# Kernel optimization log

Hardware: AMD Instinct MI355X
Metric: run time of the kernel (lower is better)

## Reference

```python
import jax, jax.numpy as jnp
import numpy as np

C = 4          # num_components
B = 2          # true batch
HEADS = 24
DIM_HEAD = 64
D = HEADS * DIM_HEAD      # 1536, attn.out_dim == query dim
CROSS = 2048              # encoder hidden dim
S = 2048                  # latent sequence length
E = 77                    # encoder sequence length
PAD = 77                  # pad_length (must equal E for the broadcast in the original code)


def setup_inputs() -> dict:
    key = jax.random.key(0)
    ks = jax.random.split(key, 12)
    w = 0.02
    return {
        "hidden_states": jax.random.normal(ks[0], (B * C, S, D), jnp.float32),
        "encoder_hidden_states": jax.random.normal(ks[1], (B * C, E, CROSS), jnp.float32),
        "Wq": jax.random.normal(ks[2], (D, D), jnp.float32) * w,
        "bq": jax.random.normal(ks[3], (D,), jnp.float32) * w,
        "Wk": jax.random.normal(ks[4], (D, CROSS), jnp.float32) * w,
        "bk": jax.random.normal(ks[5], (D,), jnp.float32) * w,
        "Wv": jax.random.normal(ks[6], (D, CROSS), jnp.float32) * w,
        "bv": jax.random.normal(ks[7], (D,), jnp.float32) * w,
        "Wo": jax.random.normal(ks[8], (D, D), jnp.float32) * w,
        "bo": jax.random.normal(ks[9], (D,), jnp.float32) * w,
        "pad_length": PAD,
    }


def reference(hidden_states, encoder_hidden_states, Wq, bq, Wk, bk, Wv, bv, Wo, bo, pad_length):
    BC, S_, D_ = hidden_states.shape
    E_ = encoder_hidden_states.shape[1]
    Bsz = BC // C
    scale = 1.0 / np.sqrt(DIM_HEAD)

    # projections (torch nn.Linear: x @ W.T + b)
    q = hidden_states @ Wq.T + bq                      # [BC, S, D]
    k = encoder_hidden_states @ Wk.T + bk              # [BC, E, D]
    v = encoder_hidden_states @ Wv.T + bv              # [BC, E, D]
    # pad branch: to_k/to_v applied to zeros -> just the bias, broadcast over pad tokens
    k_pad = jnp.broadcast_to(bk, (BC, pad_length, D_))  # [BC, PAD, D]
    v_pad = jnp.broadcast_to(bv, (BC, pad_length, D_))
    v = jnp.concatenate([v, v_pad], axis=1)            # [BC, E+PAD, D]

    # split heads
    qh = q.reshape(BC, S_, HEADS, DIM_HEAD)
    kh = k.reshape(BC, E_, HEADS, DIM_HEAD)
    kph = k_pad.reshape(BC, pad_length, HEADS, DIM_HEAD)
    vh = v.reshape(BC, E_ + pad_length, HEADS, DIM_HEAD)

    # scores: [BC, H, S, E] and [BC, H, S, PAD]
    scores = jnp.einsum("bihd,bjhd->bhij", qh, kh) * scale
    scores_pad = jnp.einsum("bihd,bjhd->bhij", qh, kph) * scale

    # component-wise softmax: view as [C, B, H, S, *], softmax over component axis 0
    scores = scores.reshape(C, Bsz, HEADS, S_, E_)
    scores_pad = scores_pad.reshape(C, Bsz, HEADS, S_, pad_length)
    w_main = jax.nn.softmax(scores, axis=0)
    w_pad = jax.nn.softmax(scores_pad, axis=0) * (C / pad_length) * (1.0 - w_main)

    w_main = w_main.reshape(BC, HEADS, S_, E_)
    w_pad = w_pad.reshape(BC, HEADS, S_, pad_length)
    weights = jnp.concatenate([w_main, w_pad], axis=-1)  # [BC, H, S, E+PAD]

    # attention @ V -> merge heads
    out = jnp.einsum("bhij,bjhd->bihd", weights, vh).reshape(BC, S_, D_)
    out = out @ Wo.T + bo   # to_out[0]; dropout is identity in eval
    return out
```

## Files before the change

kernel.cpp:

```cpp
#include <hip/hip_runtime.h>
#include <hip/hip_bf16.h>


typedef __attribute__((ext_vector_type(8))) short short8;
typedef __attribute__((ext_vector_type(4))) float f32x4;
typedef __attribute__((ext_vector_type(4))) _Float16 half4;

#define DEV __device__ __forceinline__

DEV ushort f2bf(float x) {
  __hip_bfloat16 h = __float2bfloat16(x);
  return *reinterpret_cast<ushort*>(&h);
}


__global__ __launch_bounds__(256) void cvt_f32_bf16(const float* __restrict__ in,
                                                    ushort* __restrict__ out, int n4) {
  int idx = blockIdx.x * blockDim.x + threadIdx.x;
  int stride = gridDim.x * blockDim.x;
  for (int q = idx; q < n4; q += stride) {
    float4 f = reinterpret_cast<const float4*>(in)[q];
    ushort4 o;
    o.x = f2bf(f.x); o.y = f2bf(f.y); o.z = f2bf(f.z); o.w = f2bf(f.w);
    reinterpret_cast<ushort4*>(out)[q] = o;
  }
}

__global__ __launch_bounds__(256) void cvt_pad_ehs(const float* __restrict__ in,
                                                   ushort* __restrict__ out) {
  int q = blockIdx.x * blockDim.x + threadIdx.x;
  if (q >= 640 * 2048 / 4) return;
  int r = (q * 4) >> 11;
  ushort4 o;
  if (r < 616) {
    float4 f = reinterpret_cast<const float4*>(in)[q];
    o.x = f2bf(f.x); o.y = f2bf(f.y); o.z = f2bf(f.z); o.w = f2bf(f.w);
  } else {
    o.x = 0; o.y = 0; o.z = 0; o.w = 0;
  }
  reinterpret_cast<ushort4*>(out)[q] = o;
}


template <typename OutT>
__global__ __launch_bounds__(256) void gemm_p(const ushort* __restrict__ A,
                                              const ushort* __restrict__ B,
                                              const float* __restrict__ bias,
                                              OutT* __restrict__ C, int M, int N, int K) {
  __shared__ __align__(16) ushort lds[32768];
  const int tid = threadIdx.x;
  const int lane = tid & 63;
  const int wid = tid >> 6;
  const int wr = wid >> 1, wc = wid & 1;
  const long m0 = (long)blockIdx.x * 128;
  const long n0 = (long)blockIdx.y * 128;
  const int ll = lane & 15, g = lane >> 4;
  const int swz = ll & 7;

  const int srow = wid * 8 + (lane >> 3);
  const int scol = ((lane & 7) ^ (lane >> 3)) * 8;
  const ushort* pa = A + (m0 + srow) * (long)K + scol;
  const ushort* pb = B + (n0 + srow) * (long)K + scol;
  const long qstep = 32 * (long)K;

  f32x4 acc[4][4] = {};

#define STAGE(tt, bsel)                                                                    \
  do {                                                                                     \
    const long kt_ = (long)(tt) * 64;                                                      \
    const int ab_ = (bsel) * 32768 + wid * 1024;                                           \
    _Pragma("unroll") for (int q = 0; q < 4; ++q)                                          \
        __builtin_amdgcn_global_load_lds(                                                  \
            (const __attribute__((address_space(1))) void*)(pa + kt_ + q * qstep),         \
            (__attribute__((address_space(3))) void*)((char*)lds + ab_ + q * 4096),        \
            16, 0, 0);                                                                     \
    _Pragma("unroll") for (int q = 0; q < 4; ++q)                                          \
        __builtin_amdgcn_global_load_lds(                                                  \
            (const __attribute__((address_space(1))) void*)(pb + kt_ + q * qstep),         \
            (__attribute__((address_space(3))) void*)((char*)lds + ab_ + 16384 + q * 4096),\
            16, 0, 0);                                                                     \
  } while (0)

  const int nt = K >> 6;
  STAGE(0, 0);
  STAGE(1, 1);
  asm volatile("s_waitcnt vmcnt(8)" ::: "memory");
  __builtin_amdgcn_s_barrier();

  for (int t = 0; t < nt; ++t) {
    const int buf = t & 1;
    const char* abase = (const char*)lds + buf * 32768;
    const char* bbase = abase + 16384;
    short8 af[4][2], bfr[4][2];
#pragma unroll
    for (int m = 0; m < 4; ++m)
#pragma unroll
      for (int ks = 0; ks < 2; ++ks)
        af[m][ks] = *reinterpret_cast<const short8*>(
            abase + (wr * 64 + m * 16 + ll) * 128 + (((ks * 4 + g) ^ swz) * 16));
#pragma unroll
    for (int n = 0; n < 4; ++n)
#pragma unroll
      for (int ks = 0; ks < 2; ++ks)
        bfr[n][ks] = *reinterpret_cast<const short8*>(
            bbase + (wc * 64 + n * 16 + ll) * 128 + (((ks * 4 + g) ^ swz) * 16));
    asm volatile("s_waitcnt lgkmcnt(0)" ::: "memory");
    __builtin_amdgcn_s_barrier();

    if (t < nt - 2) {
      STAGE(t + 2, buf);
      asm volatile("s_waitcnt vmcnt(8)" ::: "memory");
    } else if (t == nt - 2) {
      asm volatile("s_waitcnt vmcnt(0)" ::: "memory");
    }
    __builtin_amdgcn_sched_barrier(0);
    __builtin_amdgcn_s_setprio(1);
#pragma unroll
    for (int ks = 0; ks < 2; ++ks)
#pragma unroll
      for (int m = 0; m < 4; ++m)
#pragma unroll
        for (int n = 0; n < 4; ++n)
          acc[m][n] =
              __builtin_amdgcn_mfma_f32_16x16x32_bf16(af[m][ks], bfr[n][ks], acc[m][n], 0, 0, 0);
    __builtin_amdgcn_s_setprio(0);
    __builtin_amdgcn_s_barrier();
  }
#undef STAGE

#pragma unroll
  for (int m = 0; m < 4; ++m) {
#pragma unroll
    for (int n = 0; n < 4; ++n) {
      const int row = wr * 64 + m * 16 + g * 4;
      const int col = wc * 64 + n * 16 + ll;
      const float bias_v = bias[n0 + col];
#pragma unroll
      for (int r = 0; r < 4; ++r) {
        float val = acc[m][n][r] + bias_v;
        long off = (m0 + row + r) * (long)N + n0 + col;
        if constexpr (sizeof(OutT) == 2) {
          C[off] = (OutT)f2bf(val);
        } else {
          C[off] = val;
        }
      }
    }
  }
}


__global__ __launch_bounds__(256) void attn_v2(const ushort* __restrict__ qg,
                                               const float* __restrict__ kg,
                                               const float* __restrict__ vg,
                                               const float* __restrict__ bk,
                                               const float* __restrict__ bv,
                                               ushort* __restrict__ ao) {
  __shared__ __align__(16) ushort kl[4 * 80 * 64];
  __shared__ __align__(16) _Float16 vt[4 * 64 * 80];
  const int tid = threadIdx.x;
  const int lane = tid & 63;
  const int w = tid >> 6;
  const int h = blockIdx.y, bb = blockIdx.z;
  const int i0 = blockIdx.x * 64;

  for (int rr = tid; rr < 320; rr += 256) {
    int c = rr / 80, j = rr - c * 80;
    ushort* krow = &kl[c * 5120 + j * 64];
    _Float16* vcol = &vt[c * 5120 + j];
    const int swz = j & 7;
    if (j < 77) {
      const float* ksrc = kg + ((long)((c * 2 + bb) * 77 + j)) * 1536 + h * 64;
      const float* vsrc = vg + ((long)((c * 2 + bb) * 77 + j)) * 1536 + h * 64;
#pragma unroll
      for (int t = 0; t < 8; ++t) {
        float4 f0 = reinterpret_cast<const float4*>(ksrc)[2 * t];
        float4 f1 = reinterpret_cast<const float4*>(ksrc)[2 * t + 1];
        short8 v;
        v[0] = f2bf(f0.x); v[1] = f2bf(f0.y); v[2] = f2bf(f0.z); v[3] = f2bf(f0.w);
        v[4] = f2bf(f1.x); v[5] = f2bf(f1.y); v[6] = f2bf(f1.z); v[7] = f2bf(f1.w);
        *reinterpret_cast<short8*>(krow + (t ^ swz) * 8) = v;
      }
#pragma unroll
      for (int d = 0; d < 64; ++d) vcol[d * 80] = (_Float16)vsrc[d];
    } else if (j == 77) {
      const float* ksrc = bk + h * 64;
      const float* vsrc = bv + h * 64;
#pragma unroll
      for (int t = 0; t < 8; ++t) {
        float4 f0 = reinterpret_cast<const float4*>(ksrc)[2 * t];
        float4 f1 = reinterpret_cast<const float4*>(ksrc)[2 * t + 1];
        short8 v;
        v[0] = f2bf(f0.x); v[1] = f2bf(f0.y); v[2] = f2bf(f0.z); v[3] = f2bf(f0.w);
        v[4] = f2bf(f1.x); v[5] = f2bf(f1.y); v[6] = f2bf(f1.z); v[7] = f2bf(f1.w);
        *reinterpret_cast<short8*>(krow + (t ^ swz) * 8) = v;
      }
#pragma unroll
      for (int d = 0; d < 64; ++d) vcol[d * 80] = (_Float16)vsrc[d];
    } else {
      short8 z = {};
#pragma unroll
      for (int t = 0; t < 8; ++t) *reinterpret_cast<short8*>(krow + (t ^ swz) * 8) = z;
#pragma unroll
      for (int d = 0; d < 64; ++d) vcol[d * 80] = (_Float16)0.f;
    }
  }
  __syncthreads();

  const int ll = lane & 15, g = lane >> 4;

  f32x4 s[4][5];
#pragma unroll
  for (int c = 0; c < 4; ++c)
#pragma unroll
    for (int m = 0; m < 5; ++m) s[c][m] = (f32x4){0.f, 0.f, 0.f, 0.f};

#pragma unroll
  for (int c = 0; c < 4; ++c) {
    const ushort* qbase =
        qg + ((long)((c * 2 + bb) * 2048 + i0 + w * 16 + ll)) * 1536 + h * 64 + g * 8;
    short8 qf0 = *reinterpret_cast<const short8*>(qbase);
    short8 qf1 = *reinterpret_cast<const short8*>(qbase + 32);
#pragma unroll
    for (int m = 0; m < 5; ++m) {
      const char* base = (const char*)kl + c * 10240 + (m * 16 + ll) * 128;
      short8 a0 = *reinterpret_cast<const short8*>(base + ((g ^ (ll & 7)) * 16));
      short8 a1 = *reinterpret_cast<const short8*>(base + (((4 + g) ^ (ll & 7)) * 16));
      s[c][m] = __builtin_amdgcn_mfma_f32_16x16x32_bf16(a0, qf0, s[c][m], 0, 0, 0);
      s[c][m] = __builtin_amdgcn_mfma_f32_16x16x32_bf16(a1, qf1, s[c][m], 0, 0, 0);
    }
  }

  const float scale = 0.125f;
  float wsum0 = 0.f, wsum1 = 0.f, wsum2 = 0.f, wsum3 = 0.f;
#pragma unroll
  for (int m = 0; m < 5; ++m) {
#pragma unroll
    for (int e = 0; e < 4; ++e) {
      float x0 = s[0][m][e] * scale, x1 = s[1][m][e] * scale;
      float x2 = s[2][m][e] * scale, x3 = s[3][m][e] * scale;
      float mx = fmaxf(fmaxf(x0, x1), fmaxf(x2, x3));
      float e0 = __expf(x0 - mx), e1 = __expf(x1 - mx);
      float e2 = __expf(x2 - mx), e3 = __expf(x3 - mx);
      float inv = __fdividef(1.f, e0 + e1 + e2 + e3);
      float w0 = e0 * inv, w1 = e1 * inv, w2 = e2 * inv, w3 = e3 * inv;
      int jj = m * 16 + g * 4 + e;
      float msk = (jj < 77) ? 1.f : 0.f;
      wsum0 += w0 * msk; wsum1 += w1 * msk; wsum2 += w2 * msk; wsum3 += w3 * msk;
      s[0][m][e] = w0; s[1][m][e] = w1; s[2][m][e] = w2; s[3][m][e] = w3;
    }
  }
  wsum0 += __shfl_xor(wsum0, 16); wsum0 += __shfl_xor(wsum0, 32);
  wsum1 += __shfl_xor(wsum1, 16); wsum1 += __shfl_xor(wsum1, 32);
  wsum2 += __shfl_xor(wsum2, 16); wsum2 += __shfl_xor(wsum2, 32);
  wsum3 += __shfl_xor(wsum3, 16); wsum3 += __shfl_xor(wsum3, 32);

  const bool g3 = (g == 3);
  {
    float wsum[4] = {wsum0, wsum1, wsum2, wsum3};
#pragma unroll
    for (int c = 0; c < 4; ++c) {
      float w77 = s[c][4][1];
      float pwv = w77 * (4.0f / 77.0f) * (77.0f - wsum[c]);
      s[c][4][1] = g3 ? pwv : w77;
      s[c][4][2] = g3 ? 0.f : s[c][4][2];
      s[c][4][3] = g3 ? 0.f : s[c][4][3];
    }
  }

  half4 wf[4][5];
#pragma unroll
  for (int c = 0; c < 4; ++c)
#pragma unroll
    for (int m = 0; m < 5; ++m) {
      half4 hv;
      hv[0] = (_Float16)s[c][m][0];
      hv[1] = (_Float16)s[c][m][1];
      hv[2] = (_Float16)s[c][m][2];
      hv[3] = (_Float16)s[c][m][3];
      wf[c][m] = hv;
    }

  f32x4 o[4][4];
#pragma unroll
  for (int c = 0; c < 4; ++c)
#pragma unroll
    for (int n = 0; n < 4; ++n) o[c][n] = (f32x4){0.f, 0.f, 0.f, 0.f};

#pragma unroll
  for (int c = 0; c < 4; ++c)
#pragma unroll
    for (int m = 0; m < 5; ++m)
#pragma unroll
      for (int n = 0; n < 4; ++n) {
        half4 vf = *reinterpret_cast<const half4*>(
            &vt[c * 5120 + (n * 16 + ll) * 80 + m * 16 + g * 4]);
        o[c][n] = __builtin_amdgcn_mfma_f32_16x16x16f16(wf[c][m], vf, o[c][n], 0, 0, 0);
      }

#pragma unroll
  for (int c = 0; c < 4; ++c)
#pragma unroll
    for (int n = 0; n < 4; ++n)
#pragma unroll
      for (int r = 0; r < 4; ++r) {
        long row = (long)((c * 2 + bb) * 2048 + i0 + w * 16 + g * 4 + r);
        ao[row * 1536 + h * 64 + n * 16 + ll] = f2bf(o[c][n][r]);
      }
}


extern "C" void kernel_launch(void* const* d_in, const int* in_sizes, int n_in,
                              void* d_out, int out_size, void* d_ws, size_t ws_size,
                              hipStream_t stream) {
  (void)in_sizes; (void)n_in; (void)out_size; (void)ws_size;
  const float* hs  = (const float*)d_in[0];
  const float* ehs = (const float*)d_in[1];
  const float* Wq  = (const float*)d_in[2];
  const float* bq  = (const float*)d_in[3];
  const float* Wk  = (const float*)d_in[4];
  const float* bk  = (const float*)d_in[5];
  const float* Wv  = (const float*)d_in[6];
  const float* bv  = (const float*)d_in[7];
  const float* Wo  = (const float*)d_in[8];
  const float* bo  = (const float*)d_in[9];
  float* out = (float*)d_out;

  char* ws = (char*)d_ws;
  size_t off = 0;
  auto alloc = [&](size_t bytes) {
    char* p = ws + off;
    off += (bytes + 255) & ~(size_t)255;
    return p;
  };
  ushort* hs_bf  = (ushort*)alloc(16384UL * 1536 * 2);
  ushort* ehs_bf = (ushort*)alloc(640UL * 2048 * 2);
  ushort* Wq_bf  = (ushort*)alloc(1536UL * 1536 * 2);
  ushort* Wk_bf  = (ushort*)alloc(1536UL * 2048 * 2);
  ushort* Wv_bf  = (ushort*)alloc(1536UL * 2048 * 2);
  ushort* Wo_bf  = (ushort*)alloc(1536UL * 1536 * 2);
  ushort* q_bf   = (ushort*)alloc(16384UL * 1536 * 2);
  float*  k_f    = (float*)alloc(640UL * 1536 * 4);
  float*  v_f    = (float*)alloc(640UL * 1536 * 4);
  ushort* ao_bf  = (ushort*)alloc(16384UL * 1536 * 2);

  dim3 b256(256);
  cvt_f32_bf16<<<2048, b256, 0, stream>>>(hs, hs_bf, 16384 * 1536 / 4);
  cvt_pad_ehs<<<(640 * 2048 / 4 + 255) / 256, b256, 0, stream>>>(ehs, ehs_bf);
  cvt_f32_bf16<<<1024, b256, 0, stream>>>(Wq, Wq_bf, 1536 * 1536 / 4);
  cvt_f32_bf16<<<1024, b256, 0, stream>>>(Wk, Wk_bf, 1536 * 2048 / 4);
  cvt_f32_bf16<<<1024, b256, 0, stream>>>(Wv, Wv_bf, 1536 * 2048 / 4);
  cvt_f32_bf16<<<1024, b256, 0, stream>>>(Wo, Wo_bf, 1536 * 1536 / 4);

  gemm_p<float><<<dim3(5, 12), b256, 0, stream>>>(ehs_bf, Wk_bf, bk, k_f, 640, 1536, 2048);
  gemm_p<float><<<dim3(5, 12), b256, 0, stream>>>(ehs_bf, Wv_bf, bv, v_f, 640, 1536, 2048);
  gemm_p<ushort><<<dim3(128, 12), b256, 0, stream>>>(hs_bf, Wq_bf, bq, q_bf, 16384, 1536, 1536);
  attn_v2<<<dim3(32, 24, 2), b256, 0, stream>>>(q_bf, k_f, v_f, bk, bv, ao_bf);
  gemm_p<float><<<dim3(128, 12), b256, 0, stream>>>(ao_bf, Wo_bf, bo, out, 16384, 1536, 1536);
}
```

Baseline: 318.1 us.

## Load GEMM B operand directly from global, halve LDS, batch weight conversions

The GEMM now stages only the A tile through LDS and reads the B (weight) fragments straight from global memory into registers. This halves LDS use and sets launch bounds to allow 3 blocks per CU, aiming for higher occupancy. The four weight conversions are merged into one launch, and the K and V projections into one launch, to cut launch overhead. In exchange, every block reads B from global without LDS sharing, and those loads are not coalesced the way the staged loads were, which risks higher memory latency and traffic. The vmcnt wait counts are adjusted for the mix of direct and LDS loads.

```diff
diff --git a/kernel.cpp b/kernel.cpp
--- a/kernel.cpp
+++ b/kernel.cpp
@@ -16,6 +16,27 @@
 
 __global__ __launch_bounds__(256) void cvt_f32_bf16(const float* __restrict__ in,
                                                     ushort* __restrict__ out, int n4) {
+  int idx = blockIdx.x * blockDim.x + threadIdx.x;
+  int stride = gridDim.x * blockDim.x;
+  for (int q = idx; q < n4; q += stride) {
+    float4 f = reinterpret_cast<const float4*>(in)[q];
+    ushort4 o;
+    o.x = f2bf(f.x); o.y = f2bf(f.y); o.z = f2bf(f.z); o.w = f2bf(f.w);
+    reinterpret_cast<ushort4*>(out)[q] = o;
+  }
+}
+
+__global__ __launch_bounds__(256) void cvt_w4(const float* __restrict__ w0, ushort* __restrict__ o0, int m0,
+                                              const float* __restrict__ w1, ushort* __restrict__ o1, int m1,
+                                              const float* __restrict__ w2, ushort* __restrict__ o2, int m2,
+                                              const float* __restrict__ w3, ushort* __restrict__ o3, int m3) {
+  const float* in; ushort* out; int n4;
+  switch (blockIdx.y) {
+    case 0: in = w0; out = o0; n4 = m0; break;
+    case 1: in = w1; out = o1; n4 = m1; break;
+    case 2: in = w2; out = o2; n4 = m2; break;
+    default: in = w3; out = o3; n4 = m3; break;
+  }
   int idx = blockIdx.x * blockDim.x + threadIdx.x;
   int stride = gridDim.x * blockDim.x;
   for (int q = idx; q < n4; q += stride) {
@@ -43,11 +64,10 @@
 
 
 template <typename OutT>
-__global__ __launch_bounds__(256) void gemm_p(const ushort* __restrict__ A,
-                                              const ushort* __restrict__ B,
-                                              const float* __restrict__ bias,
-                                              OutT* __restrict__ C, int M, int N, int K) {
-  __shared__ __align__(16) ushort lds[32768];
+DEV void gemm_body(const ushort* __restrict__ A, const ushort* __restrict__ B,
+                   const float* __restrict__ bias, OutT* __restrict__ C,
+                   int M, int N, int K) {
+  __shared__ __align__(16) ushort lds[16384];
   const int tid = threadIdx.x;
   const int lane = tid & 63;
   const int wid = tid >> 6;
@@ -60,37 +80,31 @@
   const int srow = wid * 8 + (lane >> 3);
   const int scol = ((lane & 7) ^ (lane >> 3)) * 8;
   const ushort* pa = A + (m0 + srow) * (long)K + scol;
-  const ushort* pb = B + (n0 + srow) * (long)K + scol;
   const long qstep = 32 * (long)K;
+  const ushort* pB = B + (n0 + wc * 64 + ll) * (long)K + g * 8;
 
   f32x4 acc[4][4] = {};
 
-#define STAGE(tt, bsel)                                                                    \
+#define STAGEA(tt, bsel)                                                                   \
   do {                                                                                     \
     const long kt_ = (long)(tt) * 64;                                                      \
-    const int ab_ = (bsel) * 32768 + wid * 1024;                                           \
+    const int ab_ = (bsel) * 16384 + wid * 1024;                                           \
     _Pragma("unroll") for (int q = 0; q < 4; ++q)                                          \
         __builtin_amdgcn_global_load_lds(                                                  \
             (const __attribute__((address_space(1))) void*)(pa + kt_ + q * qstep),         \
             (__attribute__((address_space(3))) void*)((char*)lds + ab_ + q * 4096),        \
             16, 0, 0);                                                                     \
-    _Pragma("unroll") for (int q = 0; q < 4; ++q)                                          \
-        __builtin_amdgcn_global_load_lds(                                                  \
-            (const __attribute__((address_space(1))) void*)(pb + kt_ + q * qstep),         \
-            (__attribute__((address_space(3))) void*)((char*)lds + ab_ + 16384 + q * 4096),\
-            16, 0, 0);                                                                     \
   } while (0)
 
   const int nt = K >> 6;
-  STAGE(0, 0);
-  STAGE(1, 1);
-  asm volatile("s_waitcnt vmcnt(8)" ::: "memory");
+  STAGEA(0, 0);
+  STAGEA(1, 1);
+  asm volatile("s_waitcnt vmcnt(4)" ::: "memory");
   __builtin_amdgcn_s_barrier();
 
   for (int t = 0; t < nt; ++t) {
     const int buf = t & 1;
-    const char* abase = (const char*)lds + buf * 32768;
-    const char* bbase = abase + 16384;
+    const char* abase = (const char*)lds + buf * 16384;
     short8 af[4][2], bfr[4][2];
 #pragma unroll
     for (int m = 0; m < 4; ++m)
@@ -98,20 +112,21 @@
       for (int ks = 0; ks < 2; ++ks)
         af[m][ks] = *reinterpret_cast<const short8*>(
             abase + (wr * 64 + m * 16 + ll) * 128 + (((ks * 4 + g) ^ swz) * 16));
+    const long kb = (long)t * 64;
 #pragma unroll
     for (int n = 0; n < 4; ++n)
 #pragma unroll
       for (int ks = 0; ks < 2; ++ks)
-        bfr[n][ks] = *reinterpret_cast<const short8*>(
-            bbase + (wc * 64 + n * 16 + ll) * 128 + (((ks * 4 + g) ^ swz) * 16));
+        bfr[n][ks] = *reinterpret_cast<const short8*>(pB + (long)n * 16 * K + kb + ks * 32);
     asm volatile("s_waitcnt lgkmcnt(0)" ::: "memory");
+    __builtin_amdgcn_sched_barrier(0);
     __builtin_amdgcn_s_barrier();
 
     if (t < nt - 2) {
-      STAGE(t + 2, buf);
+      STAGEA(t + 2, buf);
+      asm volatile("s_waitcnt vmcnt(12)" ::: "memory");
+    } else if (t == nt - 2) {
       asm volatile("s_waitcnt vmcnt(8)" ::: "memory");
-    } else if (t == nt - 2) {
-      asm volatile("s_waitcnt vmcnt(0)" ::: "memory");
     }
     __builtin_amdgcn_sched_barrier(0);
     __builtin_amdgcn_s_setprio(1);
@@ -126,7 +141,7 @@
     __builtin_amdgcn_s_setprio(0);
     __builtin_amdgcn_s_barrier();
   }
-#undef STAGE
+#undef STAGEA
 
 #pragma unroll
   for (int m = 0; m < 4; ++m) {
@@ -147,6 +162,26 @@
       }
     }
   }
+}
+
+template <typename OutT>
+__global__ __launch_bounds__(256, 3) void gemm_p2(const ushort* __restrict__ A,
+                                                  const ushort* __restrict__ B,
+                                                  const float* __restrict__ bias,
+                                                  OutT* __restrict__ C, int M, int N, int K) {
+  gemm_body<OutT>(A, B, bias, C, M, N, K);
+}
+
+__global__ __launch_bounds__(256, 3) void gemm_p2_kv(const ushort* __restrict__ A,
+                                                     const ushort* __restrict__ Bk,
+                                                     const float* __restrict__ bk, float* Ck,
+                                                     const ushort* __restrict__ Bv,
+                                                     const float* __restrict__ bv, float* Cv,
+                                                     int M, int N, int K) {
+  if (blockIdx.z == 0)
+    gemm_body<float>(A, Bk, bk, Ck, M, N, K);
+  else
+    gemm_body<float>(A, Bv, bv, Cv, M, N, K);
 }
 
 
@@ -347,14 +382,14 @@
   dim3 b256(256);
   cvt_f32_bf16<<<2048, b256, 0, stream>>>(hs, hs_bf, 16384 * 1536 / 4);
   cvt_pad_ehs<<<(640 * 2048 / 4 + 255) / 256, b256, 0, stream>>>(ehs, ehs_bf);
-  cvt_f32_bf16<<<1024, b256, 0, stream>>>(Wq, Wq_bf, 1536 * 1536 / 4);
-  cvt_f32_bf16<<<1024, b256, 0, stream>>>(Wk, Wk_bf, 1536 * 2048 / 4);
-  cvt_f32_bf16<<<1024, b256, 0, stream>>>(Wv, Wv_bf, 1536 * 2048 / 4);
-  cvt_f32_bf16<<<1024, b256, 0, stream>>>(Wo, Wo_bf, 1536 * 1536 / 4);
-
-  gemm_p<float><<<dim3(5, 12), b256, 0, stream>>>(ehs_bf, Wk_bf, bk, k_f, 640, 1536, 2048);
-  gemm_p<float><<<dim3(5, 12), b256, 0, stream>>>(ehs_bf, Wv_bf, bv, v_f, 640, 1536, 2048);
-  gemm_p<ushort><<<dim3(128, 12), b256, 0, stream>>>(hs_bf, Wq_bf, bq, q_bf, 16384, 1536, 1536);
+  cvt_w4<<<dim3(768, 4), b256, 0, stream>>>(Wq, Wq_bf, 1536 * 1536 / 4,
+                                            Wk, Wk_bf, 1536 * 2048 / 4,
+                                            Wv, Wv_bf, 1536 * 2048 / 4,
+                                            Wo, Wo_bf, 1536 * 1536 / 4);
+
+  gemm_p2_kv<<<dim3(5, 12, 2), b256, 0, stream>>>(ehs_bf, Wk_bf, bk, k_f, Wv_bf, bv, v_f,
+                                                  640, 1536, 2048);
+  gemm_p2<ushort><<<dim3(128, 12), b256, 0, stream>>>(hs_bf, Wq_bf, bq, q_bf, 16384, 1536, 1536);
   attn_v2<<<dim3(32, 24, 2), b256, 0, stream>>>(q_bf, k_f, v_f, bk, bv, ao_bf);
-  gemm_p<float><<<dim3(128, 12), b256, 0, stream>>>(ao_bf, Wo_bf, bo, out, 16384, 1536, 1536);
-}
+  gemm_p2<float><<<dim3(128, 12), b256, 0, stream>>>(ao_bf, Wo_bf, bo, out, 16384, 1536, 1536);
+}
```

Measured after the change: 476.7 us. 1.5x slower.
